# Optimization experiments

Measured on AMD Instinct MI355X. Metric: run time of the kernel, lower is better.

Reference implementation:

```python
import jax, jax.numpy as jnp
import numpy as np


def setup_inputs() -> dict:
    key = jax.random.key(0)
    k1, k2 = jax.random.split(key)
    user_attributes = jax.random.normal(k1, (32, 128, 256), dtype=jnp.float32)
    image_attributes = jax.random.normal(k2, (32, 256, 256), dtype=jnp.float32)
    return {"user_attributes": user_attributes, "image_attributes": image_attributes}


def reference(user_attributes, image_attributes):
    # Math: inter[b,u,i,d] = user[b,u,d] * img[b,i,d]
    #   sum over i -> user[b,u,d] * sum_i img[b,i,d]
    #   sum over u -> img[b,i,d]  * sum_u user[b,u,d]
    # Algebraically identical to the O(U*I*D) broadcast, without materializing it.
    img_sum = jnp.sum(image_attributes, axis=1, keepdims=True)   # [B,1,D]
    user_sum = jnp.sum(user_attributes, axis=1, keepdims=True)   # [B,1,D]
    aggregated_interactions_user = user_attributes * img_sum     # [B,U,D]
    aggregated_interactions_img = image_attributes * user_sum    # [B,I,D]
    return (aggregated_interactions_user, aggregated_interactions_img)
```

## Files before the change

kernel.cpp:

```cpp
#include <hip/hip_runtime.h>

#define B 32
#define U 128
#define I 256
#define D 256

#define PU_OFF 0
#define PI_OFF (B * 4 * D)

__global__ void __launch_bounds__(256) reduce_partial_kernel(
    const float* __restrict__ user,
    const float* __restrict__ img,
    float* __restrict__ ws) {
  __shared__ float4 part[4][64];
  const int blk  = blockIdx.x;
  const int tid  = threadIdx.x;
  const int rg   = tid >> 6;
  const int lane = tid & 63;

  const float4* src4;
  float4* dst4;
  if (blk < 128) {
    const int b = blk >> 2, c = blk & 3;
    src4 = (const float4*)(user + (size_t)b * U * D) + (size_t)c * 32 * 64;
    dst4 = (float4*)(ws + PU_OFF) + (size_t)(b * 4 + c) * 64;
  } else {
    const int k = blk - 128;
    const int b = k >> 3, c = k & 7;
    src4 = (const float4*)(img + (size_t)b * I * D) + (size_t)c * 32 * 64;
    dst4 = (float4*)(ws + PI_OFF) + (size_t)(b * 8 + c) * 64;
  }

  float4 acc = make_float4(0.f, 0.f, 0.f, 0.f);
  #pragma unroll
  for (int it = 0; it < 8; ++it) {
    const float4 v = src4[(size_t)(rg * 8 + it) * 64 + lane];
    acc.x += v.x; acc.y += v.y; acc.z += v.z; acc.w += v.w;
  }
  part[rg][lane] = acc;
  __syncthreads();
  if (rg == 0) {
    const float4 a = part[0][lane];
    const float4 b4 = part[1][lane];
    const float4 c = part[2][lane];
    const float4 e = part[3][lane];
    dst4[lane] = make_float4(a.x + b4.x + c.x + e.x,
                             a.y + b4.y + c.y + e.y,
                             a.z + b4.z + c.z + e.z,
                             a.w + b4.w + c.w + e.w);
  }
}

__global__ void __launch_bounds__(256) multiply_kernel(
    const float* __restrict__ user,
    const float* __restrict__ img,
    const float* __restrict__ ws,
    float* __restrict__ out) {
  constexpr int U4  = U * D / 4;
  constexpr int I4  = I * D / 4;
  constexpr int NU4 = B * U4;
  constexpr int NI4 = B * I4;

  const int g = blockIdx.x * blockDim.x + threadIdx.x;
  const float4* u4  = (const float4*)user;
  const float4* i4  = (const float4*)img;
  const float4* pu4 = (const float4*)(ws + PU_OFF);
  const float4* pi4 = (const float4*)(ws + PI_OFF);
  float4* o4 = (float4*)out;

  if (g < NU4) {
    const int b  = g >> 13;
    const int d4 = g & 63;
    const float4* p = pi4 + (size_t)b * 8 * 64 + d4;
    float4 s = p[0];
    #pragma unroll
    for (int c = 1; c < 8; ++c) {
      const float4 t = p[(size_t)c * 64];
      s.x += t.x; s.y += t.y; s.z += t.z; s.w += t.w;
    }
    const float4 v = u4[g];
    o4[g] = make_float4(v.x * s.x, v.y * s.y, v.z * s.z, v.w * s.w);
  } else if (g < NU4 + NI4) {
    const int k  = g - NU4;
    const int b  = k >> 14;
    const int d4 = k & 63;
    const float4* p = pu4 + (size_t)b * 4 * 64 + d4;
    float4 s = p[0];
    #pragma unroll
    for (int c = 1; c < 4; ++c) {
      const float4 t = p[(size_t)c * 64];
      s.x += t.x; s.y += t.y; s.z += t.z; s.w += t.w;
    }
    const float4 v = i4[k];
    o4[NU4 + k] = make_float4(v.x * s.x, v.y * s.y, v.z * s.z, v.w * s.w);
  }
}

extern "C" void kernel_launch(void* const* d_in, const int* in_sizes, int n_in,
                              void* d_out, int out_size, void* d_ws, size_t ws_size,
                              hipStream_t stream) {
  const float* user = (const float*)d_in[0];
  const float* img  = (const float*)d_in[1];
  float* out = (float*)d_out;
  float* ws  = (float*)d_ws;

  reduce_partial_kernel<<<dim3(384), dim3(256), 0, stream>>>(user, img, ws);

  constexpr int total4 = (B * U * D + B * I * D) / 4;
  multiply_kernel<<<dim3(total4 / 256), dim3(256), 0, stream>>>(user, img, ws, out);
}
```

Before: 70.59 us.

## Fuse reduction and multiply into one kernel with redundant per-block opposite-tensor sums

Replaces the two-kernel scheme (partial reductions to workspace, then elementwise multiply) with a single kernel of 384 blocks. Each block loads its own 32-row chunk into registers, recomputes the full column sum of the opposite tensor for its batch, and writes the scaled chunk. The aim is to drop the second launch and the workspace round trip, and to let each block reuse its own registers instead of rereading its input. In exchange every block redundantly reads the whole opposite tensor for its batch, roughly 4-8x extra reads, which the block-index swizzle hopes will mostly hit in L2/MALL.

```diff
diff --git a/kernel.cpp b/kernel.cpp
--- a/kernel.cpp
+++ b/kernel.cpp
@@ -5,94 +5,74 @@
 #define I 256
 #define D 256
 
-#define PU_OFF 0
-#define PI_OFF (B * 4 * D)
-
-__global__ void __launch_bounds__(256) reduce_partial_kernel(
+__global__ void __launch_bounds__(256) fused_interaction_kernel(
     const float* __restrict__ user,
     const float* __restrict__ img,
-    float* __restrict__ ws) {
+    float* __restrict__ out) {
+  constexpr int U4b = U * D / 4;
+  constexpr int I4b = I * D / 4;
+  constexpr int NU4 = B * U4b;
+
   __shared__ float4 part[4][64];
+
   const int blk  = blockIdx.x;
+  const int unit = (blk & 7) * 48 + (blk >> 3);
+  const int b    = unit / 12;
+  const int j    = unit - b * 12;
+
   const int tid  = threadIdx.x;
   const int rg   = tid >> 6;
   const int lane = tid & 63;
 
-  const float4* src4;
-  float4* dst4;
-  if (blk < 128) {
-    const int b = blk >> 2, c = blk & 3;
-    src4 = (const float4*)(user + (size_t)b * U * D) + (size_t)c * 32 * 64;
-    dst4 = (float4*)(ws + PU_OFF) + (size_t)(b * 4 + c) * 64;
-  } else {
-    const int k = blk - 128;
-    const int b = k >> 3, c = k & 7;
-    src4 = (const float4*)(img + (size_t)b * I * D) + (size_t)c * 32 * 64;
-    dst4 = (float4*)(ws + PI_OFF) + (size_t)(b * 8 + c) * 64;
-  }
+  const float4* u4 = (const float4*)user;
+  const float4* i4 = (const float4*)img;
+  float4* o4 = (float4*)out;
+
+  const bool isUser = (j < 4);
+  const int  c      = isUser ? j : (j - 4);
+
+  const size_t ownBase = (isUser ? (size_t)b * U4b : (size_t)b * I4b)
+                       + (size_t)c * 32 * 64;
+  const float4* own = (isUser ? u4 : i4) + ownBase;
+  float4* dst = o4 + (isUser ? ownBase : (size_t)NU4 + ownBase);
+
+  float4 v[8];
+  #pragma unroll
+  for (int it = 0; it < 8; ++it)
+    v[it] = own[(size_t)(rg * 8 + it) * 64 + lane];
 
   float4 acc = make_float4(0.f, 0.f, 0.f, 0.f);
-  #pragma unroll
-  for (int it = 0; it < 8; ++it) {
-    const float4 v = src4[(size_t)(rg * 8 + it) * 64 + lane];
-    acc.x += v.x; acc.y += v.y; acc.z += v.z; acc.w += v.w;
+  if (isUser) {
+    const float4* opp = i4 + (size_t)b * I4b;
+    #pragma unroll 16
+    for (int r = rg * 64; r < rg * 64 + 64; ++r) {
+      const float4 t = opp[(size_t)r * 64 + lane];
+      acc.x += t.x; acc.y += t.y; acc.z += t.z; acc.w += t.w;
+    }
+  } else {
+    const float4* opp = u4 + (size_t)b * U4b;
+    #pragma unroll 16
+    for (int r = rg * 32; r < rg * 32 + 32; ++r) {
+      const float4 t = opp[(size_t)r * 64 + lane];
+      acc.x += t.x; acc.y += t.y; acc.z += t.z; acc.w += t.w;
+    }
   }
   part[rg][lane] = acc;
   __syncthreads();
-  if (rg == 0) {
-    const float4 a = part[0][lane];
-    const float4 b4 = part[1][lane];
-    const float4 c = part[2][lane];
-    const float4 e = part[3][lane];
-    dst4[lane] = make_float4(a.x + b4.x + c.x + e.x,
-                             a.y + b4.y + c.y + e.y,
-                             a.z + b4.z + c.z + e.z,
-                             a.w + b4.w + c.w + e.w);
-  }
-}
+  const float4 p0 = part[0][lane];
+  const float4 p1 = part[1][lane];
+  const float4 p2 = part[2][lane];
+  const float4 p3 = part[3][lane];
+  const float4 s  = make_float4(p0.x + p1.x + p2.x + p3.x,
+                                p0.y + p1.y + p2.y + p3.y,
+                                p0.z + p1.z + p2.z + p3.z,
+                                p0.w + p1.w + p2.w + p3.w);
 
-__global__ void __launch_bounds__(256) multiply_kernel(
-    const float* __restrict__ user,
-    const float* __restrict__ img,
-    const float* __restrict__ ws,
-    float* __restrict__ out) {
-  constexpr int U4  = U * D / 4;
-  constexpr int I4  = I * D / 4;
-  constexpr int NU4 = B * U4;
-  constexpr int NI4 = B * I4;
-
-  const int g = blockIdx.x * blockDim.x + threadIdx.x;
-  const float4* u4  = (const float4*)user;
-  const float4* i4  = (const float4*)img;
-  const float4* pu4 = (const float4*)(ws + PU_OFF);
-  const float4* pi4 = (const float4*)(ws + PI_OFF);
-  float4* o4 = (float4*)out;
-
-  if (g < NU4) {
-    const int b  = g >> 13;
-    const int d4 = g & 63;
-    const float4* p = pi4 + (size_t)b * 8 * 64 + d4;
-    float4 s = p[0];
-    #pragma unroll
-    for (int c = 1; c < 8; ++c) {
-      const float4 t = p[(size_t)c * 64];
-      s.x += t.x; s.y += t.y; s.z += t.z; s.w += t.w;
-    }
-    const float4 v = u4[g];
-    o4[g] = make_float4(v.x * s.x, v.y * s.y, v.z * s.z, v.w * s.w);
-  } else if (g < NU4 + NI4) {
-    const int k  = g - NU4;
-    const int b  = k >> 14;
-    const int d4 = k & 63;
-    const float4* p = pu4 + (size_t)b * 4 * 64 + d4;
-    float4 s = p[0];
-    #pragma unroll
-    for (int c = 1; c < 4; ++c) {
-      const float4 t = p[(size_t)c * 64];
-      s.x += t.x; s.y += t.y; s.z += t.z; s.w += t.w;
-    }
-    const float4 v = i4[k];
-    o4[NU4 + k] = make_float4(v.x * s.x, v.y * s.y, v.z * s.z, v.w * s.w);
+  #pragma unroll
+  for (int it = 0; it < 8; ++it) {
+    const float4 r = v[it];
+    dst[(size_t)(rg * 8 + it) * 64 + lane] =
+        make_float4(r.x * s.x, r.y * s.y, r.z * s.z, r.w * s.w);
   }
 }
 
@@ -102,10 +82,7 @@
   const float* user = (const float*)d_in[0];
   const float* img  = (const float*)d_in[1];
   float* out = (float*)d_out;
-  float* ws  = (float*)d_ws;
+  (void)d_ws; (void)ws_size;
 
-  reduce_partial_kernel<<<dim3(384), dim3(256), 0, stream>>>(user, img, ws);
-
-  constexpr int total4 = (B * U * D + B * I * D) / 4;
-  multiply_kernel<<<dim3(total4 / 256), dim3(256), 0, stream>>>(user, img, ws, out);
+  fused_interaction_kernel<<<dim3(384), dim3(256), 0, stream>>>(user, img, out);
 }
```

Result: no change. 70.40 us (-0.3%).
